# Kernel optimization log

Measured on AMD Instinct MI355X. Metric: run time of the kernel, lower is better.

Reference implementation:

```python
import jax, jax.numpy as jnp
import numpy as np

N_NODES = 100_000
N_EDGES = 800_000
IN, HID, OUT = 128, 128, 128
NTYPES = 2


def setup_inputs() -> dict:
    key = jax.random.key(0)
    ks = jax.random.split(key, 6)
    x = jax.random.normal(ks[0], (N_NODES, IN), dtype=jnp.float32)
    # nodes ordered items-then-users -> sorted type ids
    ntype = jnp.sort(jax.random.randint(ks[1], (N_NODES,), 0, NTYPES))
    src = jax.random.randint(ks[2], (N_EDGES,), 0, N_NODES)
    dst = jax.random.randint(ks[3], (N_EDGES,), 0, N_NODES)
    # TypedLinear weights: [num_types, d_in, d_out], xavier-ish scale
    W_v = jax.random.normal(ks[4], (NTYPES, IN, HID), dtype=jnp.float32) * (1.0 / np.sqrt(IN))
    W_a = jax.random.normal(ks[5], (NTYPES, HID, OUT), dtype=jnp.float32) * (1.0 / np.sqrt(HID))
    return {"x": x, "ntype": ntype, "src": src, "dst": dst, "W_v": W_v, "W_a": W_a}


def typed_linear(x, W, ntype):
    # x: [N, d_in], W: [T, d_in, d_out], ntype: [N] in [0, T)
    # T is tiny (2): compute all-type projections and select per node.
    all_proj = jnp.einsum('nd,tdh->nth', x, W)  # [N, T, d_out]
    return jnp.take_along_axis(all_proj, ntype[:, None, None], axis=1)[:, 0, :]


def reference(x, ntype, src, dst, W_v, W_a):
    # v = linear_v(x, ntype): per-type projection
    v = typed_linear(x, W_v, ntype)  # [N, HID]
    # update_all(copy_u('v','m'), sum('m','h')): scatter-sum src features to dst
    h = jax.ops.segment_sum(v[src], dst, num_segments=x.shape[0])  # [N, HID]
    # drop(linear_a(h, ntype)); dropout is identity in eval mode
    h = typed_linear(h, W_a, ntype)  # [N, OUT]
    return h
```

## Files before the change

kernel.cpp:

```cpp
#include <hip/hip_runtime.h>

#define D 128
#define SCAN_ELEMS 1024

typedef __attribute__((ext_vector_type(8))) __bf16 bf16x8;
typedef __attribute__((ext_vector_type(4))) float  f32x4;

__global__ __launch_bounds__(256) void wprep_kernel(
    const float* __restrict__ Wv, const float* __restrict__ Wa,
    __bf16* __restrict__ wt)
{
    int idx = blockIdx.x * 256 + threadIdx.x;
    int m   = idx >> 14;
    int col = (idx >> 7) & 127;
    int k   = idx & 127;
    const float* src = (m < 2) ? Wv + ((size_t)m * 128 + k) * 128 + col
                               : Wa + ((size_t)(m - 2) * 128 + k) * 128 + col;
    wt[idx] = (__bf16)(*src);
}

__global__ __launch_bounds__(256, 4) void typed_mfma_kernel(
    const float* __restrict__ X, const __bf16* __restrict__ WT,
    const int* __restrict__ ntype, float* __restrict__ Y, int n)
{
    __shared__ float lds_y[32 * 132];

    const int tix = threadIdx.x;
    const int w   = tix >> 6;
    const int l   = tix & 63;
    const int l15 = l & 15;
    const int lk  = l >> 4;
    const int bm  = blockIdx.x * 64;

    const int last = (bm + 63 < n) ? bm + 63 : n - 1;
    const int t0   = ntype[bm];
    const int t1   = ntype[last];
    const bool uni = (t0 == t1);

    for (int t = t0; t <= t1; ++t) {
        const __bf16* wb = WT + ((size_t)t << 14);
        bf16x8 wfr[4][2];
        #pragma unroll
        for (int ks = 0; ks < 4; ++ks)
            #pragma unroll
            for (int nf = 0; nf < 2; ++nf) {
                int col = w * 32 + nf * 16 + l15;
                wfr[ks][nf] = *reinterpret_cast<const bf16x8*>(
                    wb + col * 128 + ks * 32 + lk * 8);
            }

        f32x4 acc[4][2];
        #pragma unroll
        for (int rg = 0; rg < 4; ++rg)
            #pragma unroll
            for (int nf = 0; nf < 2; ++nf)
                acc[rg][nf] = (f32x4){0.f, 0.f, 0.f, 0.f};

        #pragma unroll
        for (int rg = 0; rg < 4; ++rg) {
            int row = bm + rg * 16 + l15;
            if (row > n - 1) row = n - 1;
            const float* xr = X + (size_t)row * D + lk * 8;
            #pragma unroll
            for (int ks = 0; ks < 4; ++ks) {
                float4 f0 = *reinterpret_cast<const float4*>(xr + ks * 32);
                float4 f1 = *reinterpret_cast<const float4*>(xr + ks * 32 + 4);
                bf16x8 a;
                a[0] = (__bf16)f0.x; a[1] = (__bf16)f0.y;
                a[2] = (__bf16)f0.z; a[3] = (__bf16)f0.w;
                a[4] = (__bf16)f1.x; a[5] = (__bf16)f1.y;
                a[6] = (__bf16)f1.z; a[7] = (__bf16)f1.w;
                acc[rg][0] = __builtin_amdgcn_mfma_f32_16x16x32_bf16(
                    wfr[ks][0], a, acc[rg][0], 0, 0, 0);
                acc[rg][1] = __builtin_amdgcn_mfma_f32_16x16x32_bf16(
                    wfr[ks][1], a, acc[rg][1], 0, 0, 0);
            }
        }

        #pragma unroll
        for (int ch = 0; ch < 2; ++ch) {
            __syncthreads();
            #pragma unroll
            for (int rh = 0; rh < 2; ++rh) {
                int rg = ch * 2 + rh;
                #pragma unroll
                for (int nf = 0; nf < 2; ++nf) {
                    int rloc = rh * 16 + l15;
                    int c    = w * 32 + nf * 16 + lk * 4;
                    *reinterpret_cast<float4*>(&lds_y[rloc * 132 + c]) =
                        make_float4(acc[rg][nf][0], acc[rg][nf][1],
                                    acc[rg][nf][2], acc[rg][nf][3]);
                }
            }
            __syncthreads();
            #pragma unroll
            for (int p = 0; p < 4; ++p) {
                int idx = tix + p * 256;
                int rr  = idx >> 5;
                int c4  = idx & 31;
                int row = bm + ch * 32 + rr;
                if (row < n && (uni || ntype[row] == t)) {
                    float4 val = *reinterpret_cast<const float4*>(
                        &lds_y[rr * 132 + c4 * 4]);
                    *reinterpret_cast<float4*>(&Y[(size_t)row * D + c4 * 4]) = val;
                }
            }
        }
    }
}

__global__ __launch_bounds__(256) void hist_kernel(
    const int* __restrict__ dst, int* __restrict__ counts, int ne)
{
    int stride = gridDim.x * blockDim.x;
    for (int e = blockIdx.x * blockDim.x + threadIdx.x; e < ne; e += stride)
        atomicAdd(&counts[dst[e]], 1);
}

__global__ __launch_bounds__(256) void scan1_kernel(
    const int* __restrict__ counts, int* __restrict__ offs,
    int* __restrict__ bsums, int n)
{
    __shared__ int lds[256];
    const int t    = threadIdx.x;
    const int base = blockIdx.x * SCAN_ELEMS + t * 4;

    int c[4]; int sum = 0;
    #pragma unroll
    for (int i = 0; i < 4; ++i) {
        c[i] = (base + i < n) ? counts[base + i] : 0;
        sum += c[i];
    }
    lds[t] = sum;
    __syncthreads();
    for (int off = 1; off < 256; off <<= 1) {
        int x = (t >= off) ? lds[t - off] : 0;
        __syncthreads();
        lds[t] += x;
        __syncthreads();
    }
    int run = (t == 0) ? 0 : lds[t - 1];
    #pragma unroll
    for (int i = 0; i < 4; ++i) {
        if (base + i < n) offs[base + i] = run;
        run += c[i];
    }
    if (t == 255) bsums[blockIdx.x] = lds[255];
}

__global__ __launch_bounds__(256) void scan2_kernel(int* __restrict__ bsums, int nb)
{
    __shared__ int lds[256];
    const int t    = threadIdx.x;
    const int base = t * 4;
    int c[4]; int sum = 0;
    #pragma unroll
    for (int i = 0; i < 4; ++i) {
        c[i] = (base + i < nb) ? bsums[base + i] : 0;
        sum += c[i];
    }
    lds[t] = sum;
    __syncthreads();
    for (int off = 1; off < 256; off <<= 1) {
        int x = (t >= off) ? lds[t - off] : 0;
        __syncthreads();
        lds[t] += x;
        __syncthreads();
    }
    int run = (t == 0) ? 0 : lds[t - 1];
    #pragma unroll
    for (int i = 0; i < 4; ++i) {
        if (base + i < nb) bsums[base + i] = run;
        run += c[i];
    }
}

__global__ __launch_bounds__(256) void scan3_kernel(
    int* __restrict__ offs, int* __restrict__ cursor,
    const int* __restrict__ bsums, int n)
{
    int i = blockIdx.x * blockDim.x + threadIdx.x;
    if (i < n) {
        int o = offs[i] + bsums[i / SCAN_ELEMS];
        offs[i]   = o;
        cursor[i] = o;
    }
}

__global__ __launch_bounds__(256) void place_kernel(
    const int* __restrict__ src, const int* __restrict__ dst,
    int* __restrict__ cursor, int* __restrict__ ssrc, int ne)
{
    int stride = gridDim.x * blockDim.x;
    for (int e = blockIdx.x * blockDim.x + threadIdx.x; e < ne; e += stride) {
        int d   = dst[e];
        int pos = atomicAdd(&cursor[d], 1);
        ssrc[pos] = src[e];
    }
}

__global__ __launch_bounds__(256) void gather_kernel(
    const float* __restrict__ V, const int* __restrict__ offs,
    const int* __restrict__ counts, const int* __restrict__ ssrc,
    float* __restrict__ H, int n)
{
    const int wid  = (int)((blockIdx.x * 256 + threadIdx.x) >> 6);
    const int lane = threadIdx.x & 63;
    if (wid >= n) return;

    const int beg = offs[wid];
    const int cnt = counts[wid];
    const float2* V2 = reinterpret_cast<const float2*>(V);

    float2 acc = make_float2(0.f, 0.f);
    int j = 0;
    for (; j + 1 < cnt; j += 2) {
        int s0 = ssrc[beg + j];
        int s1 = ssrc[beg + j + 1];
        float2 a = V2[(size_t)s0 * 64 + lane];
        float2 b = V2[(size_t)s1 * 64 + lane];
        acc.x += a.x + b.x;
        acc.y += a.y + b.y;
    }
    if (j < cnt) {
        int s = ssrc[beg + j];
        float2 a = V2[(size_t)s * 64 + lane];
        acc.x += a.x;
        acc.y += a.y;
    }
    reinterpret_cast<float2*>(H)[(size_t)wid * 64 + lane] = acc;
}

extern "C" void kernel_launch(void* const* d_in, const int* in_sizes, int n_in,
                              void* d_out, int out_size, void* d_ws, size_t ws_size,
                              hipStream_t stream)
{
    const float* x     = (const float*)d_in[0];
    const int*   ntype = (const int*)d_in[1];
    const int*   src   = (const int*)d_in[2];
    const int*   dst   = (const int*)d_in[3];
    const float* Wv    = (const float*)d_in[4];
    const float* Wa    = (const float*)d_in[5];

    const int n  = in_sizes[0] / D;
    const int ne = in_sizes[2];

    char* ws = (char*)d_ws;
    size_t off = 0;
    auto alloc = [&](size_t bytes) {
        void* p = ws + off;
        off += (bytes + 255) & ~(size_t)255;
        return p;
    };
    float*  v      = (float*) alloc((size_t)n * D * sizeof(float));
    __bf16* wt     = (__bf16*)alloc((size_t)4 * 128 * 128 * sizeof(__bf16));
    int*    counts = (int*)   alloc((size_t)n * sizeof(int));
    int*    offs   = (int*)   alloc((size_t)n * sizeof(int));
    int*    cursor = (int*)   alloc((size_t)n * sizeof(int));
    int*    bsums  = (int*)   alloc(1024 * sizeof(int));
    int*    ssrc   = (int*)   alloc((size_t)ne * sizeof(int));

    float* out = (float*)d_out;

    hipMemsetAsync(counts, 0, (size_t)n * sizeof(int), stream);

    wprep_kernel<<<256, 256, 0, stream>>>(Wv, Wa, wt);

    const int nblk = (n + 63) / 64;
    typed_mfma_kernel<<<nblk, 256, 0, stream>>>(x, wt, ntype, v, n);

    hist_kernel<<<1024, 256, 0, stream>>>(dst, counts, ne);
    const int nb = (n + SCAN_ELEMS - 1) / SCAN_ELEMS;
    scan1_kernel<<<nb, 256, 0, stream>>>(counts, offs, bsums, n);
    scan2_kernel<<<1, 256, 0, stream>>>(bsums, nb);
    scan3_kernel<<<(n + 255) / 256, 256, 0, stream>>>(offs, cursor, bsums, n);
    place_kernel<<<1024, 256, 0, stream>>>(src, dst, cursor, ssrc, ne);

    const int gblk = (n * 64 + 255) / 256;
    gather_kernel<<<gblk, 256, 0, stream>>>(v, offs, counts, ssrc, out, n);

    typed_mfma_kernel<<<nblk, 256, 0, stream>>>(out, wt + 2 * 128 * 128, ntype, out, n);
}
```

Baseline: 356.7 us.

## Store intermediate node features and aggregates in bf16 to halve gather traffic

The first typed projection now writes v in bf16 instead of fp32. The gather kernel reads bf16 pairs, accumulates in fp32 with a 4-way unrolled loop, and writes h in bf16 to a new workspace buffer. A new second-projection kernel reads bf16 h directly as the MFMA operand, so no fp32-to-bf16 conversion is needed there. This cuts the random-access gather bytes and the intermediate store and load traffic roughly in half, at the cost of extra rounding on v and h.

```diff
diff --git a/kernel.cpp b/kernel.cpp
--- a/kernel.cpp
+++ b/kernel.cpp
@@ -4,6 +4,8 @@
 #define SCAN_ELEMS 1024
 
 typedef __attribute__((ext_vector_type(8))) __bf16 bf16x8;
+typedef __attribute__((ext_vector_type(4))) __bf16 bf16x4;
+typedef __attribute__((ext_vector_type(2))) __bf16 bf16x2;
 typedef __attribute__((ext_vector_type(4))) float  f32x4;
 
 __global__ __launch_bounds__(256) void wprep_kernel(
@@ -19,11 +21,11 @@
     wt[idx] = (__bf16)(*src);
 }
 
-__global__ __launch_bounds__(256, 4) void typed_mfma_kernel(
+__global__ __launch_bounds__(256, 4) void typed_mfma_f32_bf16(
     const float* __restrict__ X, const __bf16* __restrict__ WT,
-    const int* __restrict__ ntype, float* __restrict__ Y, int n)
-{
-    __shared__ float lds_y[32 * 132];
+    const int* __restrict__ ntype, __bf16* __restrict__ V, int n)
+{
+    __shared__ __bf16 lds_v[32 * 136];
 
     const int tix = threadIdx.x;
     const int w   = tix >> 6;
@@ -87,6 +89,93 @@
                 for (int nf = 0; nf < 2; ++nf) {
                     int rloc = rh * 16 + l15;
                     int c    = w * 32 + nf * 16 + lk * 4;
+                    bf16x4 o;
+                    o[0] = (__bf16)acc[rg][nf][0];
+                    o[1] = (__bf16)acc[rg][nf][1];
+                    o[2] = (__bf16)acc[rg][nf][2];
+                    o[3] = (__bf16)acc[rg][nf][3];
+                    *reinterpret_cast<bf16x4*>(&lds_v[rloc * 136 + c]) = o;
+                }
+            }
+            __syncthreads();
+            #pragma unroll
+            for (int p = 0; p < 2; ++p) {
+                int idx = tix + p * 256;
+                int rr  = idx >> 4;
+                int c8  = idx & 15;
+                int row = bm + ch * 32 + rr;
+                if (row < n && (uni || ntype[row] == t)) {
+                    bf16x8 val = *reinterpret_cast<const bf16x8*>(
+                        &lds_v[rr * 136 + c8 * 8]);
+                    *reinterpret_cast<bf16x8*>(&V[(size_t)row * D + c8 * 8]) = val;
+                }
+            }
+        }
+    }
+}
+
+__global__ __launch_bounds__(256, 4) void typed_mfma_bf16_f32(
+    const __bf16* __restrict__ H, const __bf16* __restrict__ WT,
+    const int* __restrict__ ntype, float* __restrict__ Y, int n)
+{
+    __shared__ float lds_y[32 * 132];
+
+    const int tix = threadIdx.x;
+    const int w   = tix >> 6;
+    const int l   = tix & 63;
+    const int l15 = l & 15;
+    const int lk  = l >> 4;
+    const int bm  = blockIdx.x * 64;
+
+    const int last = (bm + 63 < n) ? bm + 63 : n - 1;
+    const int t0   = ntype[bm];
+    const int t1   = ntype[last];
+    const bool uni = (t0 == t1);
+
+    for (int t = t0; t <= t1; ++t) {
+        const __bf16* wb = WT + ((size_t)t << 14);
+        bf16x8 wfr[4][2];
+        #pragma unroll
+        for (int ks = 0; ks < 4; ++ks)
+            #pragma unroll
+            for (int nf = 0; nf < 2; ++nf) {
+                int col = w * 32 + nf * 16 + l15;
+                wfr[ks][nf] = *reinterpret_cast<const bf16x8*>(
+                    wb + col * 128 + ks * 32 + lk * 8);
+            }
+
+        f32x4 acc[4][2];
+        #pragma unroll
+        for (int rg = 0; rg < 4; ++rg)
+            #pragma unroll
+            for (int nf = 0; nf < 2; ++nf)
+                acc[rg][nf] = (f32x4){0.f, 0.f, 0.f, 0.f};
+
+        #pragma unroll
+        for (int rg = 0; rg < 4; ++rg) {
+            int row = bm + rg * 16 + l15;
+            if (row > n - 1) row = n - 1;
+            const __bf16* hr = H + (size_t)row * D + lk * 8;
+            #pragma unroll
+            for (int ks = 0; ks < 4; ++ks) {
+                bf16x8 a = *reinterpret_cast<const bf16x8*>(hr + ks * 32);
+                acc[rg][0] = __builtin_amdgcn_mfma_f32_16x16x32_bf16(
+                    wfr[ks][0], a, acc[rg][0], 0, 0, 0);
+                acc[rg][1] = __builtin_amdgcn_mfma_f32_16x16x32_bf16(
+                    wfr[ks][1], a, acc[rg][1], 0, 0, 0);
+            }
+        }
+
+        #pragma unroll
+        for (int ch = 0; ch < 2; ++ch) {
+            __syncthreads();
+            #pragma unroll
+            for (int rh = 0; rh < 2; ++rh) {
+                int rg = ch * 2 + rh;
+                #pragma unroll
+                for (int nf = 0; nf < 2; ++nf) {
+                    int rloc = rh * 16 + l15;
+                    int c    = w * 32 + nf * 16 + lk * 4;
                     *reinterpret_cast<float4*>(&lds_y[rloc * 132 + c]) =
                         make_float4(acc[rg][nf][0], acc[rg][nf][1],
                                     acc[rg][nf][2], acc[rg][nf][3]);
@@ -200,9 +289,9 @@
 }
 
 __global__ __launch_bounds__(256) void gather_kernel(
-    const float* __restrict__ V, const int* __restrict__ offs,
+    const __bf16* __restrict__ V, const int* __restrict__ offs,
     const int* __restrict__ counts, const int* __restrict__ ssrc,
-    float* __restrict__ H, int n)
+    __bf16* __restrict__ H, int n)
 {
     const int wid  = (int)((blockIdx.x * 256 + threadIdx.x) >> 6);
     const int lane = threadIdx.x & 63;
@@ -210,25 +299,35 @@
 
     const int beg = offs[wid];
     const int cnt = counts[wid];
-    const float2* V2 = reinterpret_cast<const float2*>(V);
-
-    float2 acc = make_float2(0.f, 0.f);
+    const unsigned int* V32 = reinterpret_cast<const unsigned int*>(V);
+
+    float ax = 0.f, ay = 0.f;
     int j = 0;
-    for (; j + 1 < cnt; j += 2) {
+    for (; j + 3 < cnt; j += 4) {
         int s0 = ssrc[beg + j];
         int s1 = ssrc[beg + j + 1];
-        float2 a = V2[(size_t)s0 * 64 + lane];
-        float2 b = V2[(size_t)s1 * 64 + lane];
-        acc.x += a.x + b.x;
-        acc.y += a.y + b.y;
-    }
-    if (j < cnt) {
+        int s2 = ssrc[beg + j + 2];
+        int s3 = ssrc[beg + j + 3];
+        unsigned int u0 = V32[(size_t)s0 * 64 + lane];
+        unsigned int u1 = V32[(size_t)s1 * 64 + lane];
+        unsigned int u2 = V32[(size_t)s2 * 64 + lane];
+        unsigned int u3 = V32[(size_t)s3 * 64 + lane];
+        ax += __uint_as_float(u0 << 16) + __uint_as_float(u1 << 16)
+            + __uint_as_float(u2 << 16) + __uint_as_float(u3 << 16);
+        ay += __uint_as_float(u0 & 0xffff0000u) + __uint_as_float(u1 & 0xffff0000u)
+            + __uint_as_float(u2 & 0xffff0000u) + __uint_as_float(u3 & 0xffff0000u);
+    }
+    for (; j < cnt; ++j) {
         int s = ssrc[beg + j];
-        float2 a = V2[(size_t)s * 64 + lane];
-        acc.x += a.x;
-        acc.y += a.y;
-    }
-    reinterpret_cast<float2*>(H)[(size_t)wid * 64 + lane] = acc;
+        unsigned int u = V32[(size_t)s * 64 + lane];
+        ax += __uint_as_float(u << 16);
+        ay += __uint_as_float(u & 0xffff0000u);
+    }
+
+    bf16x2 o;
+    o[0] = (__bf16)ax;
+    o[1] = (__bf16)ay;
+    reinterpret_cast<bf16x2*>(H)[(size_t)wid * 64 + lane] = o;
 }
 
 extern "C" void kernel_launch(void* const* d_in, const int* in_sizes, int n_in,
@@ -252,7 +351,8 @@
         off += (bytes + 255) & ~(size_t)255;
         return p;
     };
-    float*  v      = (float*) alloc((size_t)n * D * sizeof(float));
+    __bf16* v      = (__bf16*)alloc((size_t)n * D * sizeof(__bf16));
+    __bf16* h      = (__bf16*)alloc((size_t)n * D * sizeof(__bf16));
     __bf16* wt     = (__bf16*)alloc((size_t)4 * 128 * 128 * sizeof(__bf16));
     int*    counts = (int*)   alloc((size_t)n * sizeof(int));
     int*    offs   = (int*)   alloc((size_t)n * sizeof(int));
@@ -267,7 +367,7 @@
     wprep_kernel<<<256, 256, 0, stream>>>(Wv, Wa, wt);
 
     const int nblk = (n + 63) / 64;
-    typed_mfma_kernel<<<nblk, 256, 0, stream>>>(x, wt, ntype, v, n);
+    typed_mfma_f32_bf16<<<nblk, 256, 0, stream>>>(x, wt, ntype, v, n);
 
     hist_kernel<<<1024, 256, 0, stream>>>(dst, counts, ne);
     const int nb = (n + SCAN_ELEMS - 1) / SCAN_ELEMS;
@@ -277,7 +377,7 @@
     place_kernel<<<1024, 256, 0, stream>>>(src, dst, cursor, ssrc, ne);
 
     const int gblk = (n * 64 + 255) / 256;
-    gather_kernel<<<gblk, 256, 0, stream>>>(v, offs, counts, ssrc, out, n);
-
-    typed_mfma_kernel<<<nblk, 256, 0, stream>>>(out, wt + 2 * 128 * 128, ntype, out, n);
-}
+    gather_kernel<<<gblk, 256, 0, stream>>>(v, offs, counts, ssrc, h, n);
+
+    typed_mfma_bf16_f32<<<nblk, 256, 0, stream>>>(h, wt + 2 * 128 * 128, ntype, out, n);
+}
```

Result: faster. 304.5 us (-14.6%).
